# Performance work log

Measured on AMD Instinct MI355X. Metric: run time of the kernel, lower is better.

## Reference

```python
import jax, jax.numpy as jnp
import numpy as np

B, S, D, H = 2, 4096, 768, 12
HD = D // H  # head_dim = 64


def setup_inputs() -> dict:
    key = jax.random.key(0)
    ks = jax.random.split(key, 12)
    s = 0.02
    inp = {
        'q': jax.random.normal(ks[0], (B, S, D), jnp.float32),
        'k': jax.random.normal(ks[1], (B, S, D), jnp.float32),
        'v': jax.random.normal(ks[2], (B, S, D), jnp.float32),
        # True = masked position (filled with -inf); causal mask, broadcastable
        'mask': jnp.triu(jnp.ones((S, S), jnp.bool_), k=1)[None, None],
        'Wq': jax.random.normal(ks[3], (D, D), jnp.float32) * s,
        'bq': jnp.zeros((D,), jnp.float32),
        'Wk': jax.random.normal(ks[4], (D, D), jnp.float32) * s,
        'bk': jnp.zeros((D,), jnp.float32),
        'Wv': jax.random.normal(ks[5], (D, D), jnp.float32) * s,
        'bv': jnp.zeros((D,), jnp.float32),
        'Wo': jax.random.normal(ks[6], (D, D), jnp.float32) * s,
        'bo': jnp.zeros((D,), jnp.float32),
    }
    return inp


def _split_heads(x):
    # [B, S, D] -> [B, H, S, HD]
    return x.reshape(B, S, H, HD).transpose(0, 2, 1, 3)


def reference(q, k, v, mask, Wq, bq, Wk, bk, Wv, bv, Wo, bo):
    # per-head linear projections (torch Linear: x @ W.T + b)
    qh = _split_heads(q @ Wq.T + bq)
    kh = _split_heads(k @ Wk.T + bk)
    vh = _split_heads(v @ Wv.T + bv)
    scale = 1.0 / np.sqrt(HD).astype(np.float32)
    # naive full [B, H, S, S] attention scores (module materializes these)
    wei = jnp.einsum('bhqd,bhkd->bhqk', qh, kh) * scale
    wei = jnp.where(mask, -jnp.inf, wei)
    attn = jax.nn.softmax(wei, axis=-1)
    feats = jnp.einsum('bhqk,bhkd->bhqd', attn, vh)
    # concat heads: [B, H, S, HD] -> [B, S, D]
    out = feats.transpose(0, 2, 1, 3).reshape(B, S, D)
    return out @ Wo.T + bo
```

## Files before the change

kernel.cpp:

```cpp
#include <hip/hip_runtime.h>
#include <math.h>

#define B_  2
#define S_  4096
#define D_  768
#define H_  12
#define HD_ 64

using bf16x8  = __attribute__((ext_vector_type(8))) __bf16;
using f32x4   = __attribute__((ext_vector_type(4))) float;
using ushort8 = __attribute__((ext_vector_type(8))) unsigned short;
using uintv2  = __attribute__((ext_vector_type(2))) unsigned;
using uintv4  = __attribute__((ext_vector_type(4))) unsigned;

__device__ __forceinline__ unsigned short f2b(float f) {
    union { float f; unsigned u; } x; x.f = f;
    unsigned r = x.u + 0x7fffu + ((x.u >> 16) & 1u);
    return (unsigned short)(r >> 16);
}
__device__ __forceinline__ unsigned pk2(float x, float y) {
    unsigned ux = __builtin_bit_cast(unsigned, x) + 0x8000u;
    unsigned uy = __builtin_bit_cast(unsigned, y) + 0x8000u;
    return (uy & 0xFFFF0000u) | (ux >> 16);
}
__device__ __forceinline__ unsigned cvtpk(float lo, float hi) {
    unsigned r;
    asm("v_cvt_pk_bf16_f32 %0, %1, %2" : "=v"(r) : "v"(lo), "v"(hi));
    return r;
}
__device__ __forceinline__ uintv2 xpose_pair(unsigned x, unsigned y) {
    uintv2 s = __builtin_amdgcn_permlane32_swap(x, y, false, false);
    return __builtin_amdgcn_permlane16_swap(s[0], s[1], false, false);
}

__global__ __launch_bounds__(256)
void w_convert(const float* __restrict__ Wq, const float* __restrict__ Wk,
               const float* __restrict__ Wv, const float* __restrict__ Wo,
               unsigned short* __restrict__ Wb)
{
    const int z = blockIdx.y;
    const float* src = (z == 0) ? Wq : (z == 1) ? Wk : (z == 2) ? Wv : Wo;
    unsigned short* dst = Wb + (size_t)z * (D_ * D_);
    int idx = blockIdx.x * 256 + threadIdx.x;
    const float4 a = *(const float4*)(src + (size_t)idx * 8);
    const float4 b = *(const float4*)(src + (size_t)idx * 8 + 4);
    uint4 o;
    o.x = pk2(a.x, a.y); o.y = pk2(a.z, a.w);
    o.z = pk2(b.x, b.y); o.w = pk2(b.z, b.w);
    *(uint4*)(dst + (size_t)idx * 8) = o;
}

__global__ __launch_bounds__(256, 2)
void qkv_gemm(const float* __restrict__ q, const float* __restrict__ k,
              const float* __restrict__ v,
              const unsigned short* __restrict__ Wb,
              const float* __restrict__ bq, const float* __restrict__ bk,
              const float* __restrict__ bv,
              unsigned short* __restrict__ Qp, unsigned short* __restrict__ Kp,
              unsigned short* __restrict__ Vt)
{
    constexpr int BM = 128, BN = 256, BK = 32, LDP = 40, NK = D_ / BK;
    const int lin = blockIdx.x;
    const int xcd = lin & 7, s = lin >> 3;
    const int z  = s / 24, rr = s % 24;
    const int bn = rr >> 3;
    const int bm = xcd * 8 + (rr & 7);

    const float* A    = (z == 0) ? q  : (z == 1) ? k  : v;
    const unsigned short* W = Wb + (size_t)z * (D_ * D_);
    const float* bias = (z == 0) ? bq : (z == 1) ? bk : bv;

    __shared__ __align__(16) unsigned short As[2][BM * LDP];
    __shared__ __align__(16) unsigned short Bs[2][BN * LDP];

    const int tid = threadIdx.x;
    const int w = tid >> 6, lane = tid & 63, lr = lane & 15, lg = lane >> 4;
    const int wm = (w >> 1) * 64, wn = (w & 1) * 128;

    const int arow = tid >> 3, ac4 = (tid & 7) * 4;
    const int brow = tid >> 2, bc8 = (tid & 3) * 8;
    const float* Abase = A + (size_t)(bm * BM + arow) * D_ + ac4;
    const unsigned short* Wbase = W + (size_t)(bn * BN + brow) * D_ + bc8;

    float4 ap[4]; ushort8 bp[4];

    for (int t = 0; t < 4; ++t) ap[t] = *(const float4*)(Abase + (size_t)t * 32 * D_);
    for (int t = 0; t < 4; ++t) bp[t] = *(const ushort8*)(Wbase + (size_t)t * 64 * D_);
    for (int t = 0; t < 4; ++t)
        *(uint2*)&As[0][(arow + t * 32) * LDP + ac4] =
            make_uint2(pk2(ap[t].x, ap[t].y), pk2(ap[t].z, ap[t].w));
    for (int t = 0; t < 4; ++t)
        *(ushort8*)&Bs[0][(brow + t * 64) * LDP + bc8] = bp[t];
    __syncthreads();

    f32x4 acc[4][8] = {};

    for (int it = 0; it < NK; ++it) {
        const int cur = it & 1;
        const int k2 = ((it + 1 < NK) ? it + 1 : it) * BK;
        for (int t = 0; t < 4; ++t) ap[t] = *(const float4*)(Abase + k2 + (size_t)t * 32 * D_);
        for (int t = 0; t < 4; ++t) bp[t] = *(const ushort8*)(Wbase + k2 + (size_t)t * 64 * D_);

        bf16x8 af[4], bfr[8];
        for (int i = 0; i < 4; ++i) af[i]  = *(const bf16x8*)&As[cur][(wm + i * 16 + lr) * LDP + lg * 8];
        for (int j = 0; j < 8; ++j) bfr[j] = *(const bf16x8*)&Bs[cur][(wn + j * 16 + lr) * LDP + lg * 8];
        for (int i = 0; i < 4; ++i)
            for (int j = 0; j < 8; ++j)
                acc[i][j] = __builtin_amdgcn_mfma_f32_16x16x32_bf16(af[i], bfr[j], acc[i][j], 0, 0, 0);

        const int nxt = cur ^ 1;
        for (int t = 0; t < 4; ++t)
            *(uint2*)&As[nxt][(arow + t * 32) * LDP + ac4] =
                make_uint2(pk2(ap[t].x, ap[t].y), pk2(ap[t].z, ap[t].w));
        for (int t = 0; t < 4; ++t)
            *(ushort8*)&Bs[nxt][(brow + t * 64) * LDP + bc8] = bp[t];
        __syncthreads();
    }

    if (z == 2) {
        for (int j = 0; j < 8; ++j) {
            const int col = bn * BN + wn + j * 16 + lr;
            const int hh = col >> 6, dd = col & 63;
            const float bv_ = bias[col];
            for (int i = 0; i < 4; ++i) {
                const int s_g = bm * BM + wm + i * 16 + lg * 4;
                const int bb = s_g >> 12, s_in = s_g & 4095;
                unsigned short e0 = f2b(acc[i][j][0] + bv_);
                unsigned short e1 = f2b(acc[i][j][1] + bv_);
                unsigned short e2 = f2b(acc[i][j][2] + bv_);
                unsigned short e3 = f2b(acc[i][j][3] + bv_);
                *(uint2*)(Vt + ((size_t)((bb * H_ + hh) * HD_ + dd)) * S_ + s_in) =
                    make_uint2((unsigned)e0 | ((unsigned)e1 << 16),
                               (unsigned)e2 | ((unsigned)e3 << 16));
            }
        }
    } else {
        unsigned short* C = (z == 0) ? Qp : Kp;
        const float qscale = 0.18033688011112042f;
        for (int i = 0; i < 4; ++i) {
            int row0 = bm * BM + wm + i * 16 + lg * 4;
            for (int j = 0; j < 8; ++j) {
                int col = bn * BN + wn + j * 16 + lr;
                float bv_ = bias[col];
                for (int r = 0; r < 4; ++r) {
                    float val = acc[i][j][r] + bv_;
                    if (z == 0) val *= qscale;
                    C[(size_t)(row0 + r) * D_ + col] = f2b(val);
                }
            }
        }
    }
}

__global__ __launch_bounds__(256)
void o_gemm(const unsigned short* __restrict__ Ai, const unsigned short* __restrict__ W,
            const float* __restrict__ bias, float* __restrict__ C)
{
    constexpr int BM = 64, BN = 128, BK = 32, LDP = 40, NK = D_ / BK;
    __shared__ __align__(16) unsigned short As[2][BM * LDP];
    __shared__ __align__(16) unsigned short Bs[2][BN * LDP];

    const int lin = blockIdx.x;
    const int xcd = lin & 7, s = lin >> 3;
    const int bn = s >> 4;
    const int bm = xcd * 16 + (s & 15);

    const int tid = threadIdx.x;
    const int w = tid >> 6, lane = tid & 63, lr = lane & 15, lg = lane >> 4;
    const int wm = (w >> 1) * 32, wn = (w & 1) * 64;

    const int arow = tid >> 2, ac8 = (tid & 3) * 8;
    const unsigned short* Abase = Ai + (size_t)(bm * BM + arow) * D_ + ac8;
    const unsigned short* Wbase = W + (size_t)(bn * BN + arow) * D_ + ac8;

    ushort8 apre, bpre[2];
    apre = *(const ushort8*)(Abase);
    for (int t = 0; t < 2; ++t) bpre[t] = *(const ushort8*)(Wbase + (size_t)t * 64 * D_);
    *(ushort8*)&As[0][arow * LDP + ac8] = apre;
    for (int t = 0; t < 2; ++t)
        *(ushort8*)&Bs[0][(arow + t * 64) * LDP + ac8] = bpre[t];
    __syncthreads();

    f32x4 acc[2][4] = {};

    for (int it = 0; it < NK; ++it) {
        const int cur = it & 1;
        const int k2 = ((it + 1 < NK) ? it + 1 : it) * BK;
        apre = *(const ushort8*)(Abase + k2);
        for (int t = 0; t < 2; ++t) bpre[t] = *(const ushort8*)(Wbase + k2 + (size_t)t * 64 * D_);

        bf16x8 af[2], bfr[4];
        for (int i = 0; i < 2; ++i) af[i]  = *(const bf16x8*)&As[cur][(wm + i * 16 + lr) * LDP + lg * 8];
        for (int j = 0; j < 4; ++j) bfr[j] = *(const bf16x8*)&Bs[cur][(wn + j * 16 + lr) * LDP + lg * 8];
        for (int i = 0; i < 2; ++i)
            for (int j = 0; j < 4; ++j)
                acc[i][j] = __builtin_amdgcn_mfma_f32_16x16x32_bf16(af[i], bfr[j], acc[i][j], 0, 0, 0);

        const int nxt = cur ^ 1;
        *(ushort8*)&As[nxt][arow * LDP + ac8] = apre;
        for (int t = 0; t < 2; ++t)
            *(ushort8*)&Bs[nxt][(arow + t * 64) * LDP + ac8] = bpre[t];
        __syncthreads();
    }

    for (int i = 0; i < 2; ++i) {
        int row0 = bm * BM + wm + i * 16 + lg * 4;
        for (int j = 0; j < 4; ++j) {
            int col = bn * BN + wn + j * 16 + lr;
            float bv_ = bias[col];
            for (int r = 0; r < 4; ++r)
                C[(size_t)(row0 + r) * D_ + col] = acc[i][j][r] + bv_;
        }
    }
}

__global__ __launch_bounds__(256)
void attn_kernel(const unsigned short* __restrict__ Qp,
                 const unsigned short* __restrict__ Kp,
                 const unsigned short* __restrict__ Vt,
                 unsigned short* __restrict__ feats)
{
    __shared__ __align__(16) unsigned short Ks[2][64 * 72];
    __shared__ __align__(16) unsigned short Vs[2][64 * 72];

    const int tid = threadIdx.x;
    const int lin = blockIdx.x + gridDim.x * blockIdx.y;
    const int xcd = lin & 7, idx = lin >> 3;
    const int bhl = idx >> 5;
    const int i   = idx & 31;
    int p;
    if (bhl == 0)      p = i;
    else if (bhl == 1) p = (i + 16) & 31;
    else               p = (i < 16) ? (31 - 2 * i) : (62 - 2 * i);
    const int bh  = xcd * 3 + bhl;
    const int b = bh / H_, h = bh % H_;
    const int w = tid >> 6, lane = tid & 63, lr = lane & 15, lg = lane >> 4;

    const int qtA = 63 - p, qtB = p;

    bf16x8 ones;
    for (int j = 0; j < 8; ++j) ones[j] = (__bf16)1.0f;

    const size_t kbase = ((size_t)b * S_) * D_ + h * HD_;
    const size_t vbase = ((size_t)bh * HD_) * S_;

    const size_t qbA = ((size_t)(b * S_ + qtA * 64 + w * 16 + lr)) * D_ + h * HD_;
    const size_t qbB = ((size_t)(b * S_ + qtB * 64 + w * 16 + lr)) * D_ + h * HD_;
    bf16x8 qfA0 = *(const bf16x8*)(Qp + qbA + lg * 8);
    bf16x8 qfA1 = *(const bf16x8*)(Qp + qbA + 32 + lg * 8);
    bf16x8 qfB0 = *(const bf16x8*)(Qp + qbB + lg * 8);
    bf16x8 qfB1 = *(const bf16x8*)(Qp + qbB + 32 + lg * 8);

    f32x4 oA[4] = {}, oB[4] = {};
    f32x4 lA = {0.f, 0.f, 0.f, 0.f}, lB = {0.f, 0.f, 0.f, 0.f};

    const int nst = qtA + 1;

    const int srow = tid >> 3, sc8 = (tid & 7) * 8;
    const unsigned short* kpt = Kp + kbase + (size_t)srow * D_ + sc8;
    const unsigned short* vpt = Vt + vbase + (size_t)srow * S_ + sc8;
    unsigned short* KsW0 = &Ks[0][srow * 72 + sc8];
    unsigned short* VsW0 = &Vs[0][srow * 72 + sc8];
    unsigned short* KsW1 = &Ks[1][srow * 72 + sc8];
    unsigned short* VsW1 = &Vs[1][srow * 72 + sc8];

    {
        ushort8 a0 = *(const ushort8*)(kpt);
        ushort8 a1 = *(const ushort8*)(kpt + (size_t)32 * D_);
        ushort8 a2 = *(const ushort8*)(vpt);
        ushort8 a3 = *(const ushort8*)(vpt + (size_t)32 * S_);
        *(ushort8*)KsW0            = a0;
        *(ushort8*)(KsW0 + 32*72)  = a1;
        *(ushort8*)VsW0            = a2;
        *(ushort8*)(VsW0 + 32*72)  = a3;
    }
    __syncthreads();

    for (int kb = 0; kb < nst; ++kb) {
        const bool bAct = (kb <= qtB);
        const int cur = kb & 1;
        const unsigned short* Kc = Ks[cur];
        const unsigned short* Vc = Vs[cur];

        const int kb2 = (kb + 1 < nst) ? kb + 1 : kb;
        const unsigned short* kp2 = kpt + (size_t)kb2 * 64 * D_;
        const unsigned short* vp2 = vpt + (size_t)kb2 * 64;
        ushort8 kr0 = *(const ushort8*)(kp2);
        ushort8 kr1 = *(const ushort8*)(kp2 + (size_t)32 * D_);
        ushort8 vr0 = *(const ushort8*)(vp2);
        ushort8 vr1 = *(const ushort8*)(vp2 + (size_t)32 * S_);

        bf16x8 kf[4][2], vf[4][2];
        for (int n = 0; n < 4; ++n) {
            kf[n][0] = *(const bf16x8*)&Kc[(n * 16 + lr) * 72 + lg * 8];
            kf[n][1] = *(const bf16x8*)&Kc[(n * 16 + lr) * 72 + 32 + lg * 8];
        }
        for (int n = 0; n < 4; ++n) {
            vf[n][0] = *(const bf16x8*)&Vc[(n * 16 + lr) * 72 + lg * 8];
            vf[n][1] = *(const bf16x8*)&Vc[(n * 16 + lr) * 72 + 32 + lg * 8];
        }

        bf16x8 pfA0, pfA1, pfB0, pfB1;

        {
            f32x4 st[4];
            for (int n = 0; n < 4; ++n) {
                f32x4 s = {0.f, 0.f, 0.f, 0.f};
                s = __builtin_amdgcn_mfma_f32_16x16x32_bf16(kf[n][0], qfA0, s, 0, 0, 0);
                s = __builtin_amdgcn_mfma_f32_16x16x32_bf16(kf[n][1], qfA1, s, 0, 0, 0);
                st[n] = s;
            }
            if (kb == qtA) {
                for (int n = 0; n < 4; ++n)
                    for (int r = 0; r < 4; ++r)
                        if (n * 16 + lg * 4 + r > w * 16 + lr) st[n][r] = -INFINITY;
            }
            unsigned a_[4][2];
            for (int n = 0; n < 4; ++n) {
                float e0 = __builtin_amdgcn_exp2f(st[n][0]);
                float e1 = __builtin_amdgcn_exp2f(st[n][1]);
                float e2 = __builtin_amdgcn_exp2f(st[n][2]);
                float e3 = __builtin_amdgcn_exp2f(st[n][3]);
                a_[n][0] = cvtpk(e0, e1);
                a_[n][1] = cvtpk(e2, e3);
            }
            uintv2 p00 = xpose_pair(a_[0][0], a_[1][0]);
            uintv2 p01 = xpose_pair(a_[0][1], a_[1][1]);
            uintv2 p10 = xpose_pair(a_[2][0], a_[3][0]);
            uintv2 p11 = xpose_pair(a_[2][1], a_[3][1]);
            uintv4 w0 = {p00[0], p01[0], p00[1], p01[1]};
            uintv4 w1 = {p10[0], p11[0], p10[1], p11[1]};
            pfA0 = __builtin_bit_cast(bf16x8, w0);
            pfA1 = __builtin_bit_cast(bf16x8, w1);
        }
        if (bAct) {
            f32x4 st[4];
            for (int n = 0; n < 4; ++n) {
                f32x4 s = {0.f, 0.f, 0.f, 0.f};
                s = __builtin_amdgcn_mfma_f32_16x16x32_bf16(kf[n][0], qfB0, s, 0, 0, 0);
                s = __builtin_amdgcn_mfma_f32_16x16x32_bf16(kf[n][1], qfB1, s, 0, 0, 0);
                st[n] = s;
            }
            if (kb == qtB) {
                for (int n = 0; n < 4; ++n)
                    for (int r = 0; r < 4; ++r)
                        if (n * 16 + lg * 4 + r > w * 16 + lr) st[n][r] = -INFINITY;
            }
            unsigned a_[4][2];
            for (int n = 0; n < 4; ++n) {
                float e0 = __builtin_amdgcn_exp2f(st[n][0]);
                float e1 = __builtin_amdgcn_exp2f(st[n][1]);
                float e2 = __builtin_amdgcn_exp2f(st[n][2]);
                float e3 = __builtin_amdgcn_exp2f(st[n][3]);
                a_[n][0] = cvtpk(e0, e1);
                a_[n][1] = cvtpk(e2, e3);
            }
            uintv2 p00 = xpose_pair(a_[0][0], a_[1][0]);
            uintv2 p01 = xpose_pair(a_[0][1], a_[1][1]);
            uintv2 p10 = xpose_pair(a_[2][0], a_[3][0]);
            uintv2 p11 = xpose_pair(a_[2][1], a_[3][1]);
            uintv4 w0 = {p00[0], p01[0], p00[1], p01[1]};
            uintv4 w1 = {p10[0], p11[0], p10[1], p11[1]};
            pfB0 = __builtin_bit_cast(bf16x8, w0);
            pfB1 = __builtin_bit_cast(bf16x8, w1);
        }

        {
            for (int n = 0; n < 4; ++n) {
                oA[n] = __builtin_amdgcn_mfma_f32_16x16x32_bf16(vf[n][0], pfA0, oA[n], 0, 0, 0);
                oA[n] = __builtin_amdgcn_mfma_f32_16x16x32_bf16(vf[n][1], pfA1, oA[n], 0, 0, 0);
            }
            lA = __builtin_amdgcn_mfma_f32_16x16x32_bf16(ones, pfA0, lA, 0, 0, 0);
            lA = __builtin_amdgcn_mfma_f32_16x16x32_bf16(ones, pfA1, lA, 0, 0, 0);
        }
        if (bAct) {
            for (int n = 0; n < 4; ++n) {
                oB[n] = __builtin_amdgcn_mfma_f32_16x16x32_bf16(vf[n][0], pfB0, oB[n], 0, 0, 0);
                oB[n] = __builtin_amdgcn_mfma_f32_16x16x32_bf16(vf[n][1], pfB1, oB[n], 0, 0, 0);
            }
            lB = __builtin_amdgcn_mfma_f32_16x16x32_bf16(ones, pfB0, lB, 0, 0, 0);
            lB = __builtin_amdgcn_mfma_f32_16x16x32_bf16(ones, pfB1, lB, 0, 0, 0);
        }

        if (cur == 0) {
            *(ushort8*)KsW1            = kr0;
            *(ushort8*)(KsW1 + 32*72)  = kr1;
            *(ushort8*)VsW1            = vr0;
            *(ushort8*)(VsW1 + 32*72)  = vr1;
        } else {
            *(ushort8*)KsW0            = kr0;
            *(ushort8*)(KsW0 + 32*72)  = kr1;
            *(ushort8*)VsW0            = vr0;
            *(ushort8*)(VsW0 + 32*72)  = vr1;
        }
        __syncthreads();
    }

    {
        const float inv = 1.0f / lA[0];
        const size_t obase = ((size_t)(b * S_ + qtA * 64 + w * 16 + lr)) * D_ + h * HD_;
        for (int n = 0; n < 4; ++n) {
            unsigned short e0 = f2b(oA[n][0] * inv), e1 = f2b(oA[n][1] * inv);
            unsigned short e2 = f2b(oA[n][2] * inv), e3 = f2b(oA[n][3] * inv);
            *(uint2*)(feats + obase + n * 16 + lg * 4) =
                make_uint2((unsigned)e0 | ((unsigned)e1 << 16),
                           (unsigned)e2 | ((unsigned)e3 << 16));
        }
    }
    {
        const float inv = 1.0f / lB[0];
        const size_t obase = ((size_t)(b * S_ + qtB * 64 + w * 16 + lr)) * D_ + h * HD_;
        for (int n = 0; n < 4; ++n) {
            unsigned short e0 = f2b(oB[n][0] * inv), e1 = f2b(oB[n][1] * inv);
            unsigned short e2 = f2b(oB[n][2] * inv), e3 = f2b(oB[n][3] * inv);
            *(uint2*)(feats + obase + n * 16 + lg * 4) =
                make_uint2((unsigned)e0 | ((unsigned)e1 << 16),
                           (unsigned)e2 | ((unsigned)e3 << 16));
        }
    }
}

extern "C" void kernel_launch(void* const* d_in, const int* in_sizes, int n_in,
                              void* d_out, int out_size, void* d_ws, size_t ws_size,
                              hipStream_t stream) {
    const float* q  = (const float*)d_in[0];
    const float* k  = (const float*)d_in[1];
    const float* v  = (const float*)d_in[2];
    const float* Wq = (const float*)d_in[4];
    const float* bq = (const float*)d_in[5];
    const float* Wk = (const float*)d_in[6];
    const float* bk = (const float*)d_in[7];
    const float* Wv = (const float*)d_in[8];
    const float* bv = (const float*)d_in[9];
    const float* Wo = (const float*)d_in[10];
    const float* bo = (const float*)d_in[11];
    float* out = (float*)d_out;

    const size_t npro = (size_t)B_ * S_ * D_;
    const size_t nw   = (size_t)D_ * D_;
    unsigned short* Qp    = (unsigned short*)d_ws;
    unsigned short* Kp    = Qp + npro;
    unsigned short* feats = Kp + npro;
    unsigned short* Vt    = feats + npro;
    unsigned short* Wb    = Vt + npro;

    dim3 blk(256);
    w_convert<<<dim3(288, 4), blk, 0, stream>>>(Wq, Wk, Wv, Wo, Wb);
    qkv_gemm<<<dim3(576), blk, 0, stream>>>(q, k, v, Wb, bq, bk, bv,
                                            Qp, Kp, Vt);
    attn_kernel<<<dim3(32, B_ * H_), blk, 0, stream>>>(Qp, Kp, Vt, feats);
    o_gemm<<<dim3(768), blk, 0, stream>>>(feats, Wb + 3 * nw, bo, out);
}
```

Measured before the change: 349.3 us.

## Split attention warps 2x2 over queries and keys with an LDS reduction

The four warps in each attention block are regrouped into a 2x2 grid. Each warp now handles 32 query rows against half of the 64-key tile, instead of 16 query rows against the full tile. This halves each warp's K and V fragment reads from LDS per step while keeping the MFMA count the same. The two key-halves' partial outputs and row sums are then combined through LDS (reusing the K/V buffers) before normalisation and store. It also adds a launch_bounds occupancy hint of 3, which raises register pressure from the doubled accumulators and adds an extra sync plus reduction epilogue.

New measurement: 326.5 us. 6.5% less time.

```diff
diff --git a/kernel.cpp b/kernel.cpp
--- a/kernel.cpp
+++ b/kernel.cpp
@@ -214,7 +214,7 @@
     }
 }
 
-__global__ __launch_bounds__(256)
+__global__ __launch_bounds__(256, 3)
 void attn_kernel(const unsigned short* __restrict__ Qp,
                  const unsigned short* __restrict__ Kp,
                  const unsigned short* __restrict__ Vt,
@@ -227,14 +227,15 @@
     const int lin = blockIdx.x + gridDim.x * blockIdx.y;
     const int xcd = lin & 7, idx = lin >> 3;
     const int bhl = idx >> 5;
-    const int i   = idx & 31;
+    const int ii  = idx & 31;
     int p;
-    if (bhl == 0)      p = i;
-    else if (bhl == 1) p = (i + 16) & 31;
-    else               p = (i < 16) ? (31 - 2 * i) : (62 - 2 * i);
+    if (bhl == 0)      p = ii;
+    else if (bhl == 1) p = (ii + 16) & 31;
+    else               p = (ii < 16) ? (31 - 2 * ii) : (62 - 2 * ii);
     const int bh  = xcd * 3 + bhl;
     const int b = bh / H_, h = bh % H_;
     const int w = tid >> 6, lane = tid & 63, lr = lane & 15, lg = lane >> 4;
+    const int wi = w >> 1, wj = w & 1;
 
     const int qtA = 63 - p, qtB = p;
 
@@ -244,15 +245,18 @@
     const size_t kbase = ((size_t)b * S_) * D_ + h * HD_;
     const size_t vbase = ((size_t)bh * HD_) * S_;
 
-    const size_t qbA = ((size_t)(b * S_ + qtA * 64 + w * 16 + lr)) * D_ + h * HD_;
-    const size_t qbB = ((size_t)(b * S_ + qtB * 64 + w * 16 + lr)) * D_ + h * HD_;
-    bf16x8 qfA0 = *(const bf16x8*)(Qp + qbA + lg * 8);
-    bf16x8 qfA1 = *(const bf16x8*)(Qp + qbA + 32 + lg * 8);
-    bf16x8 qfB0 = *(const bf16x8*)(Qp + qbB + lg * 8);
-    bf16x8 qfB1 = *(const bf16x8*)(Qp + qbB + 32 + lg * 8);
-
-    f32x4 oA[4] = {}, oB[4] = {};
-    f32x4 lA = {0.f, 0.f, 0.f, 0.f}, lB = {0.f, 0.f, 0.f, 0.f};
+    bf16x8 qfA[2][2], qfB[2][2];
+    for (int c = 0; c < 2; ++c) {
+        const size_t qA = ((size_t)(b * S_ + qtA * 64 + wi * 32 + c * 16 + lr)) * D_ + h * HD_;
+        const size_t qB = ((size_t)(b * S_ + qtB * 64 + wi * 32 + c * 16 + lr)) * D_ + h * HD_;
+        for (int hh = 0; hh < 2; ++hh) {
+            qfA[c][hh] = *(const bf16x8*)(Qp + qA + hh * 32 + lg * 8);
+            qfB[c][hh] = *(const bf16x8*)(Qp + qB + hh * 32 + lg * 8);
+        }
+    }
+
+    f32x4 oA[4][2] = {}, oB[4][2] = {};
+    f32x4 lA[2] = {}, lB[2] = {};
 
     const int nst = qtA + 1;
 
@@ -290,96 +294,84 @@
         ushort8 vr0 = *(const ushort8*)(vp2);
         ushort8 vr1 = *(const ushort8*)(vp2 + (size_t)32 * S_);
 
-        bf16x8 kf[4][2], vf[4][2];
-        for (int n = 0; n < 4; ++n) {
-            kf[n][0] = *(const bf16x8*)&Kc[(n * 16 + lr) * 72 + lg * 8];
-            kf[n][1] = *(const bf16x8*)&Kc[(n * 16 + lr) * 72 + 32 + lg * 8];
-        }
-        for (int n = 0; n < 4; ++n) {
-            vf[n][0] = *(const bf16x8*)&Vc[(n * 16 + lr) * 72 + lg * 8];
-            vf[n][1] = *(const bf16x8*)&Vc[(n * 16 + lr) * 72 + 32 + lg * 8];
-        }
-
-        bf16x8 pfA0, pfA1, pfB0, pfB1;
+        bf16x8 kf[2][2];
+        for (int m = 0; m < 2; ++m) {
+            kf[m][0] = *(const bf16x8*)&Kc[(wj * 32 + m * 16 + lr) * 72 + lg * 8];
+            kf[m][1] = *(const bf16x8*)&Kc[(wj * 32 + m * 16 + lr) * 72 + 32 + lg * 8];
+        }
+
+        bf16x8 pfA[2], pfB[2];
 
         {
-            f32x4 st[4];
-            for (int n = 0; n < 4; ++n) {
-                f32x4 s = {0.f, 0.f, 0.f, 0.f};
-                s = __builtin_amdgcn_mfma_f32_16x16x32_bf16(kf[n][0], qfA0, s, 0, 0, 0);
-                s = __builtin_amdgcn_mfma_f32_16x16x32_bf16(kf[n][1], qfA1, s, 0, 0, 0);
-                st[n] = s;
-            }
+            f32x4 st[2][2];
+            for (int m = 0; m < 2; ++m)
+                for (int c = 0; c < 2; ++c) {
+                    f32x4 s = {0.f, 0.f, 0.f, 0.f};
+                    s = __builtin_amdgcn_mfma_f32_16x16x32_bf16(kf[m][0], qfA[c][0], s, 0, 0, 0);
+                    s = __builtin_amdgcn_mfma_f32_16x16x32_bf16(kf[m][1], qfA[c][1], s, 0, 0, 0);
+                    st[m][c] = s;
+                }
             if (kb == qtA) {
-                for (int n = 0; n < 4; ++n)
-                    for (int r = 0; r < 4; ++r)
-                        if (n * 16 + lg * 4 + r > w * 16 + lr) st[n][r] = -INFINITY;
-            }
-            unsigned a_[4][2];
-            for (int n = 0; n < 4; ++n) {
-                float e0 = __builtin_amdgcn_exp2f(st[n][0]);
-                float e1 = __builtin_amdgcn_exp2f(st[n][1]);
-                float e2 = __builtin_amdgcn_exp2f(st[n][2]);
-                float e3 = __builtin_amdgcn_exp2f(st[n][3]);
-                a_[n][0] = cvtpk(e0, e1);
-                a_[n][1] = cvtpk(e2, e3);
-            }
-            uintv2 p00 = xpose_pair(a_[0][0], a_[1][0]);
-            uintv2 p01 = xpose_pair(a_[0][1], a_[1][1]);
-            uintv2 p10 = xpose_pair(a_[2][0], a_[3][0]);
-            uintv2 p11 = xpose_pair(a_[2][1], a_[3][1]);
-            uintv4 w0 = {p00[0], p01[0], p00[1], p01[1]};
-            uintv4 w1 = {p10[0], p11[0], p10[1], p11[1]};
-            pfA0 = __builtin_bit_cast(bf16x8, w0);
-            pfA1 = __builtin_bit_cast(bf16x8, w1);
+                for (int m = 0; m < 2; ++m)
+                    for (int c = 0; c < 2; ++c)
+                        for (int r = 0; r < 4; ++r)
+                            if (wj * 32 + m * 16 + lg * 4 + r > wi * 32 + c * 16 + lr)
+                                st[m][c][r] = -INFINITY;
+            }
+            for (int c = 0; c < 2; ++c) {
+                unsigned a0_ = cvtpk(__builtin_amdgcn_exp2f(st[0][c][0]), __builtin_amdgcn_exp2f(st[0][c][1]));
+                unsigned a1_ = cvtpk(__builtin_amdgcn_exp2f(st[0][c][2]), __builtin_amdgcn_exp2f(st[0][c][3]));
+                unsigned b0_ = cvtpk(__builtin_amdgcn_exp2f(st[1][c][0]), __builtin_amdgcn_exp2f(st[1][c][1]));
+                unsigned b1_ = cvtpk(__builtin_amdgcn_exp2f(st[1][c][2]), __builtin_amdgcn_exp2f(st[1][c][3]));
+                uintv2 p0 = xpose_pair(a0_, b0_);
+                uintv2 p1 = xpose_pair(a1_, b1_);
+                uintv4 wrd = {p0[0], p1[0], p0[1], p1[1]};
+                pfA[c] = __builtin_bit_cast(bf16x8, wrd);
+            }
         }
         if (bAct) {
-            f32x4 st[4];
-            for (int n = 0; n < 4; ++n) {
-                f32x4 s = {0.f, 0.f, 0.f, 0.f};
-                s = __builtin_amdgcn_mfma_f32_16x16x32_bf16(kf[n][0], qfB0, s, 0, 0, 0);
-                s = __builtin_amdgcn_mfma_f32_16x16x32_bf16(kf[n][1], qfB1, s, 0, 0, 0);
-                st[n] = s;
-            }
+            f32x4 st[2][2];
+            for (int m = 0; m < 2; ++m)
+                for (int c = 0; c < 2; ++c) {
+                    f32x4 s = {0.f, 0.f, 0.f, 0.f};
+                    s = __builtin_amdgcn_mfma_f32_16x16x32_bf16(kf[m][0], qfB[c][0], s, 0, 0, 0);
+                    s = __builtin_amdgcn_mfma_f32_16x16x32_bf16(kf[m][1], qfB[c][1], s, 0, 0, 0);
+                    st[m][c] = s;
+                }
             if (kb == qtB) {
-                for (int n = 0; n < 4; ++n)
-                    for (int r = 0; r < 4; ++r)
-                        if (n * 16 + lg * 4 + r > w * 16 + lr) st[n][r] = -INFINITY;
-            }
-            unsigned a_[4][2];
-            for (int n = 0; n < 4; ++n) {
-                float e0 = __builtin_amdgcn_exp2f(st[n][0]);
-                float e1 = __builtin_amdgcn_exp2f(st[n][1]);
-                float e2 = __builtin_amdgcn_exp2f(st[n][2]);
-                float e3 = __builtin_amdgcn_exp2f(st[n][3]);
-                a_[n][0] = cvtpk(e0, e1);
-                a_[n][1] = cvtpk(e2, e3);
-            }
-            uintv2 p00 = xpose_pair(a_[0][0], a_[1][0]);
-            uintv2 p01 = xpose_pair(a_[0][1], a_[1][1]);
-            uintv2 p10 = xpose_pair(a_[2][0], a_[3][0]);
-            uintv2 p11 = xpose_pair(a_[2][1], a_[3][1]);
-            uintv4 w0 = {p00[0], p01[0], p00[1], p01[1]};
-            uintv4 w1 = {p10[0], p11[0], p10[1], p11[1]};
-            pfB0 = __builtin_bit_cast(bf16x8, w0);
-            pfB1 = __builtin_bit_cast(bf16x8, w1);
-        }
-
-        {
-            for (int n = 0; n < 4; ++n) {
-                oA[n] = __builtin_amdgcn_mfma_f32_16x16x32_bf16(vf[n][0], pfA0, oA[n], 0, 0, 0);
-                oA[n] = __builtin_amdgcn_mfma_f32_16x16x32_bf16(vf[n][1], pfA1, oA[n], 0, 0, 0);
-            }
-            lA = __builtin_amdgcn_mfma_f32_16x16x32_bf16(ones, pfA0, lA, 0, 0, 0);
-            lA = __builtin_amdgcn_mfma_f32_16x16x32_bf16(ones, pfA1, lA, 0, 0, 0);
-        }
+                for (int m = 0; m < 2; ++m)
+                    for (int c = 0; c < 2; ++c)
+                        for (int r = 0; r < 4; ++r)
+                            if (wj * 32 + m * 16 + lg * 4 + r > wi * 32 + c * 16 + lr)
+                                st[m][c][r] = -INFINITY;
+            }
+            for (int c = 0; c < 2; ++c) {
+                unsigned a0_ = cvtpk(__builtin_amdgcn_exp2f(st[0][c][0]), __builtin_amdgcn_exp2f(st[0][c][1]));
+                unsigned a1_ = cvtpk(__builtin_amdgcn_exp2f(st[0][c][2]), __builtin_amdgcn_exp2f(st[0][c][3]));
+                unsigned b0_ = cvtpk(__builtin_amdgcn_exp2f(st[1][c][0]), __builtin_amdgcn_exp2f(st[1][c][1]));
+                unsigned b1_ = cvtpk(__builtin_amdgcn_exp2f(st[1][c][2]), __builtin_amdgcn_exp2f(st[1][c][3]));
+                uintv2 p0 = xpose_pair(a0_, b0_);
+                uintv2 p1 = xpose_pair(a1_, b1_);
+                uintv4 wrd = {p0[0], p1[0], p0[1], p1[1]};
+                pfB[c] = __builtin_bit_cast(bf16x8, wrd);
+            }
+        }
+
+        bf16x8 vf[4];
+        for (int n = 0; n < 4; ++n)
+            vf[n] = *(const bf16x8*)&Vc[(n * 16 + lr) * 72 + wj * 32 + lg * 8];
+
+        for (int n = 0; n < 4; ++n)
+            for (int c = 0; c < 2; ++c)
+                oA[n][c] = __builtin_amdgcn_mfma_f32_16x16x32_bf16(vf[n], pfA[c], oA[n][c], 0, 0, 0);
+        for (int c = 0; c < 2; ++c)
+            lA[c] = __builtin_amdgcn_mfma_f32_16x16x32_bf16(ones, pfA[c], lA[c], 0, 0, 0);
         if (bAct) {
-            for (int n = 0; n < 4; ++n) {
-                oB[n] = __builtin_amdgcn_mfma_f32_16x16x32_bf16(vf[n][0], pfB0, oB[n], 0, 0, 0);
-                oB[n] = __builtin_amdgcn_mfma_f32_16x16x32_bf16(vf[n][1], pfB1, oB[n], 0, 0, 0);
-            }
-            lB = __builtin_amdgcn_mfma_f32_16x16x32_bf16(ones, pfB0, lB, 0, 0, 0);
-            lB = __builtin_amdgcn_mfma_f32_16x16x32_bf16(ones, pfB1, lB, 0, 0, 0);
+            for (int n = 0; n < 4; ++n)
+                for (int c = 0; c < 2; ++c)
+                    oB[n][c] = __builtin_amdgcn_mfma_f32_16x16x32_bf16(vf[n], pfB[c], oB[n][c], 0, 0, 0);
+            for (int c = 0; c < 2; ++c)
+                lB[c] = __builtin_amdgcn_mfma_f32_16x16x32_bf16(ones, pfB[c], lB[c], 0, 0, 0);
         }
 
         if (cur == 0) {
@@ -396,26 +388,47 @@
         __syncthreads();
     }
 
-    {
-        const float inv = 1.0f / lA[0];
-        const size_t obase = ((size_t)(b * S_ + qtA * 64 + w * 16 + lr)) * D_ + h * HD_;
-        for (int n = 0; n < 4; ++n) {
-            unsigned short e0 = f2b(oA[n][0] * inv), e1 = f2b(oA[n][1] * inv);
-            unsigned short e2 = f2b(oA[n][2] * inv), e3 = f2b(oA[n][3] * inv);
-            *(uint2*)(feats + obase + n * 16 + lg * 4) =
-                make_uint2((unsigned)e0 | ((unsigned)e1 << 16),
-                           (unsigned)e2 | ((unsigned)e3 << 16));
-        }
-    }
-    {
-        const float inv = 1.0f / lB[0];
-        const size_t obase = ((size_t)(b * S_ + qtB * 64 + w * 16 + lr)) * D_ + h * HD_;
-        for (int n = 0; n < 4; ++n) {
-            unsigned short e0 = f2b(oB[n][0] * inv), e1 = f2b(oB[n][1] * inv);
-            unsigned short e2 = f2b(oB[n][2] * inv), e3 = f2b(oB[n][3] * inv);
-            *(uint2*)(feats + obase + n * 16 + lg * 4) =
-                make_uint2((unsigned)e0 | ((unsigned)e1 << 16),
-                           (unsigned)e2 | ((unsigned)e3 << 16));
+    float* redA = (float*)&Ks[0][0];
+    float* redB = (float*)&Vs[0][0];
+    if (wj == 1) {
+        for (int n = 0; n < 4; ++n)
+            for (int c = 0; c < 2; ++c) {
+                *(f32x4*)(redA + ((wi * 8 + n * 2 + c) * 64 + lane) * 4) = oA[n][c];
+                *(f32x4*)(redB + ((wi * 8 + n * 2 + c) * 64 + lane) * 4) = oB[n][c];
+            }
+        for (int c = 0; c < 2; ++c) {
+            redA[4096 + wi * 128 + c * 64 + lane] = lA[c][0];
+            redB[4096 + wi * 128 + c * 64 + lane] = lB[c][0];
+        }
+    }
+    __syncthreads();
+    if (wj == 0) {
+        for (int n = 0; n < 4; ++n)
+            for (int c = 0; c < 2; ++c) {
+                oA[n][c] += *(const f32x4*)(redA + ((wi * 8 + n * 2 + c) * 64 + lane) * 4);
+                oB[n][c] += *(const f32x4*)(redB + ((wi * 8 + n * 2 + c) * 64 + lane) * 4);
+            }
+        for (int c = 0; c < 2; ++c) {
+            const float invA = 1.0f / (lA[c][0] + redA[4096 + wi * 128 + c * 64 + lane]);
+            const size_t obaseA =
+                ((size_t)(b * S_ + qtA * 64 + wi * 32 + c * 16 + lr)) * D_ + h * HD_;
+            for (int n = 0; n < 4; ++n) {
+                unsigned short e0 = f2b(oA[n][c][0] * invA), e1 = f2b(oA[n][c][1] * invA);
+                unsigned short e2 = f2b(oA[n][c][2] * invA), e3 = f2b(oA[n][c][3] * invA);
+                *(uint2*)(feats + obaseA + n * 16 + lg * 4) =
+                    make_uint2((unsigned)e0 | ((unsigned)e1 << 16),
+                               (unsigned)e2 | ((unsigned)e3 << 16));
+            }
+            const float invB = 1.0f / (lB[c][0] + redB[4096 + wi * 128 + c * 64 + lane]);
+            const size_t obaseB =
+                ((size_t)(b * S_ + qtB * 64 + wi * 32 + c * 16 + lr)) * D_ + h * HD_;
+            for (int n = 0; n < 4; ++n) {
+                unsigned short e0 = f2b(oB[n][c][0] * invB), e1 = f2b(oB[n][c][1] * invB);
+                unsigned short e2 = f2b(oB[n][c][2] * invB), e3 = f2b(oB[n][c][3] * invB);
+                *(uint2*)(feats + obaseB + n * 16 + lg * 4) =
+                    make_uint2((unsigned)e0 | ((unsigned)e1 << 16),
+                               (unsigned)e2 | ((unsigned)e3 << 16));
+            }
         }
     }
 }
```
